# Performance work log

Hardware: AMD Instinct MI355X
Metric: run time of the kernel (lower is better)

The kernel has to match this reference:

```python
import jax, jax.numpy as jnp
import numpy as np

N = 65536          # nodes
E = N * 7          # edges (avg_degree = n_edge_type = 7)
C_IN = 128
C_OUT = 128
N_EDGE_TYPE = 7
N_NODE_TYPE = 5
FEAT = C_IN + N_NODE_TYPE  # 133, channels after one-hot concat


def setup_inputs() -> dict:
    key = jax.random.key(0)
    k1, k2, k3, k4, k5 = jax.random.split(key, 5)
    x = jax.random.normal(k1, (N, C_IN), dtype=jnp.float32)
    edge_idx = jax.random.randint(k2, (2, E), 0, N, dtype=jnp.int64)
    edge_type = jax.random.randint(k3, (E,), 0, N_EDGE_TYPE, dtype=jnp.int64)
    node_type = jax.random.randint(k4, (N,), 0, N_NODE_TYPE, dtype=jnp.int64)
    # uniform init a la module's reset_parameters
    fan_in = 7 * C_IN
    fan_out = 7 * C_OUT
    a = np.sqrt(3.0) * np.sqrt(2.0 / (fan_in + fan_out))
    weights = jax.random.uniform(k5, (N_EDGE_TYPE * FEAT, C_OUT), dtype=jnp.float32,
                                 minval=-a, maxval=a)
    return {"x": x, "edge_idx": edge_idx, "edge_type": edge_type,
            "node_type": node_type, "weights": weights}


def reference(x, edge_idx, edge_type, node_type, weights):
    # one-hot node type concat (n_node_type > 1 branch)
    one_hot = jax.nn.one_hot(node_type, N_NODE_TYPE, dtype=x.dtype)
    xa = jnp.concatenate([x, one_hot], axis=1)          # [N, FEAT]
    row, col = edge_idx[0], edge_idx[1]
    seg = row * N_EDGE_TYPE + edge_type                 # [E]
    gathered = xa[col]                                  # [E, FEAT]
    num_seg = N * N_EDGE_TYPE
    sums = jax.ops.segment_sum(gathered, seg, num_segments=num_seg)
    cnt = jax.ops.segment_sum(jnp.ones((E,), dtype=xa.dtype), seg, num_segments=num_seg)
    col_data = sums / jnp.maximum(cnt, 1.0)[:, None]    # scatter_mean
    # overwrite self-loop slot (last edge type) with node's own features
    self_idx = jnp.arange(N, dtype=jnp.int64) * N_EDGE_TYPE + (N_EDGE_TYPE - 1)
    col_data = col_data.at[self_idx].set(xa)
    out = col_data.reshape(N, N_EDGE_TYPE * FEAT) @ weights  # [N, C_OUT]
    return out
```

## Files before the change

### kernel.cpp

```cpp
#include <hip/hip_runtime.h>
#include <hip/hip_bf16.h>

#define N_NODES 65536
#define N_EDGES (N_NODES * 7)
#define NSEG    (N_NODES * 7)
#define CAP     12
#define ZROW    65536

typedef short short8 __attribute__((ext_vector_type(8)));
typedef float f32x4  __attribute__((ext_vector_type(4)));

__device__ __forceinline__ unsigned short f2bf(float f) {
    return __builtin_bit_cast(unsigned short, (__bf16)f);
}
__device__ __forceinline__ unsigned pack2(float lo, float hi) {
    return (unsigned)f2bf(lo) | ((unsigned)f2bf(hi) << 16);
}
__device__ __forceinline__ float bflo(unsigned d) { return __uint_as_float(d << 16); }
__device__ __forceinline__ float bfhi(unsigned d) { return __uint_as_float(d & 0xffff0000u); }

__global__ __launch_bounds__(256) void k_big(const float* __restrict__ x,
                                             const int* __restrict__ eidx,
                                             const int* __restrict__ etype,
                                             const int* __restrict__ ntype,
                                             const float* __restrict__ W,
                                             unsigned short* __restrict__ xb,
                                             unsigned short* __restrict__ wb,
                                             unsigned* __restrict__ seg32,
                                             unsigned short* __restrict__ scol) {
    int i = blockIdx.x * 256 + threadIdx.x;

    if (i < N_EDGES) {
        int t = etype[i];
        if (t < 6) {
            int r = eidx[i];
            int c = eidx[N_EDGES + i];
            int u = ntype[c];
            unsigned seg = (unsigned)r * 7u + (unsigned)t;
            unsigned inc = 1u | (1u << (7 + 5 * u));
            unsigned old = atomicAdd(&seg32[seg], inc);
            unsigned slot = old & 0x7fu;
            if (slot < CAP) scol[seg * CAP + slot] = (unsigned short)c;
        }
    }

    {
        int row = i >> 4, mm = i & 15;
        const f32x4* p = reinterpret_cast<const f32x4*>(x + (size_t)row * 128 + mm * 8);
        f32x4 v0 = p[0], v1 = p[1];
        uint4 w;
        w.x = pack2(v0[0], v0[1]); w.y = pack2(v0[2], v0[3]);
        w.z = pack2(v1[0], v1[1]); w.w = pack2(v1[2], v1[3]);
        reinterpret_cast<uint4*>(xb)[i] = w;
    }

    if (i < 16) reinterpret_cast<uint4*>(xb + (size_t)ZROW * 128)[i] = (uint4){0u, 0u, 0u, 0u};

    if (i < 143360) {
        int j    = i & 7;
        int lane = (i >> 3) & 63;
        int cb   = (i >> 9) & 7;
        int tkc  = i >> 12;
        int kc   = tkc % 5;
        int t    = tkc / 5;
        int k = kc * 32 + ((lane >> 4) << 3) + j;
        int c = cb * 16 + (lane & 15);
        float v = (k < 133) ? W[(t * 133 + k) * 128 + c] : 0.0f;
        wb[i] = f2bf(v);
    }
}

__global__ __launch_bounds__(512, 4) void k_main(const unsigned short* __restrict__ xb,
                                                 const int* __restrict__ ntype,
                                                 const unsigned* __restrict__ seg32,
                                                 const unsigned short* __restrict__ scol,
                                                 const unsigned short* __restrict__ wb,
                                                 float* __restrict__ out) {
    __shared__ unsigned short sA[7 * 32 * 168];

    const int tid  = threadIdx.x;
    const int lane = tid & 63;
    const int wid  = tid >> 6;
    const int n0   = blockIdx.x * 32;
    const int r    = tid >> 4;
    const int m    = tid & 15;
    const int n    = n0 + r;

    for (int i = tid; i < 7 * 32 * 12; i += 512) {
        int row = i / 12, j = i - row * 12;
        reinterpret_cast<unsigned*>(sA)[row * 84 + 68 + j] = 0u;
    }

    unsigned sv[6], c_t[6];
    uint2 q2[6];
    #pragma unroll
    for (int t = 0; t < 6; ++t) {
        sv[t]  = seg32[n * 7 + t];
        c_t[t] = sv[t] & 0x7fu;
        q2[t]  = *reinterpret_cast<const uint2*>(scol + ((size_t)n * 7 + t) * CAP);
    }

    short8 xA[6], xB[6], xS;
    #pragma unroll
    for (int t = 0; t < 6; ++t) {
        unsigned cA = (c_t[t] >= 1u) ? (q2[t].x & 0xffffu) : (unsigned)ZROW;
        unsigned cB = (c_t[t] >= 2u) ? (q2[t].x >> 16)     : (unsigned)ZROW;
        xA[t] = *reinterpret_cast<const short8*>(xb + (size_t)cA * 128 + m * 8);
        xB[t] = *reinterpret_cast<const short8*>(xb + (size_t)cB * 128 + m * 8);
    }
    xS = *reinterpret_cast<const short8*>(xb + (size_t)n * 128 + m * 8);
    const int ntS = ntype[n];

    #pragma unroll
    for (int t = 0; t < 6; ++t) {
        const unsigned cntv = c_t[t];
        const float inv = (cntv > 1u) ? __builtin_amdgcn_rcpf((float)cntv) : 1.0f;

        uint4 a4 = *reinterpret_cast<const uint4*>(&xA[t]);
        uint4 b4 = *reinterpret_cast<const uint4*>(&xB[t]);
        float a[8];
        a[0] = bflo(a4.x) + bflo(b4.x); a[1] = bfhi(a4.x) + bfhi(b4.x);
        a[2] = bflo(a4.y) + bflo(b4.y); a[3] = bfhi(a4.y) + bfhi(b4.y);
        a[4] = bflo(a4.z) + bflo(b4.z); a[5] = bfhi(a4.z) + bfhi(b4.z);
        a[6] = bflo(a4.w) + bflo(b4.w); a[7] = bfhi(a4.w) + bfhi(b4.w);

        if (cntv >= 3u) {
            const unsigned ce = (cntv < (unsigned)CAP) ? cntv : (unsigned)CAP;
            {
                unsigned c2 = q2[t].y & 0xffffu;
                short8 v = *reinterpret_cast<const short8*>(xb + (size_t)c2 * 128 + m * 8);
                uint4 v4 = *reinterpret_cast<const uint4*>(&v);
                a[0] += bflo(v4.x); a[1] += bfhi(v4.x);
                a[2] += bflo(v4.y); a[3] += bfhi(v4.y);
                a[4] += bflo(v4.z); a[5] += bfhi(v4.z);
                a[6] += bflo(v4.w); a[7] += bfhi(v4.w);
            }
            if (ce >= 4u) {
                unsigned c3 = q2[t].y >> 16;
                short8 v = *reinterpret_cast<const short8*>(xb + (size_t)c3 * 128 + m * 8);
                uint4 v4 = *reinterpret_cast<const uint4*>(&v);
                a[0] += bflo(v4.x); a[1] += bfhi(v4.x);
                a[2] += bflo(v4.y); a[3] += bfhi(v4.y);
                a[4] += bflo(v4.z); a[5] += bfhi(v4.z);
                a[6] += bflo(v4.w); a[7] += bfhi(v4.w);
                const size_t segbase = ((size_t)n * 7 + t) * CAP;
                for (unsigned e = 4; e < ce; ++e) {
                    unsigned c = scol[segbase + e];
                    short8 ve = *reinterpret_cast<const short8*>(xb + (size_t)c * 128 + m * 8);
                    uint4 v4e = *reinterpret_cast<const uint4*>(&ve);
                    a[0] += bflo(v4e.x); a[1] += bfhi(v4e.x);
                    a[2] += bflo(v4e.y); a[3] += bfhi(v4e.y);
                    a[4] += bflo(v4e.z); a[5] += bfhi(v4e.z);
                    a[6] += bflo(v4e.w); a[7] += bfhi(v4e.w);
                }
            }
        }

        uint4 w;
        w.x = pack2(a[0] * inv, a[1] * inv); w.y = pack2(a[2] * inv, a[3] * inv);
        w.z = pack2(a[4] * inv, a[5] * inv); w.w = pack2(a[6] * inv, a[7] * inv);
        *reinterpret_cast<uint4*>(sA + (t * 32 + r) * 168 + m * 8) = w;

        if (m < 4) {
            int i0 = 2 * m, i1 = 2 * m + 1;
            float g0 = (i0 < 5) ? (float)((sv[t] >> (7 + 5 * i0)) & 31u) : 0.f;
            float g1 = (i1 < 5) ? (float)((sv[t] >> (7 + 5 * i1)) & 31u) : 0.f;
            reinterpret_cast<unsigned*>(sA)[(t * 32 + r) * 84 + 64 + m] =
                pack2(g0 * inv, g1 * inv);
        }
    }

    *reinterpret_cast<uint4*>(sA + (6 * 32 + r) * 168 + m * 8) =
        *reinterpret_cast<const uint4*>(&xS);
    if (m < 4) {
        float g0 = (ntS == 2 * m) ? 1.f : 0.f;
        float g1 = (ntS == 2 * m + 1) ? 1.f : 0.f;
        reinterpret_cast<unsigned*>(sA)[(6 * 32 + r) * 84 + 64 + m] = pack2(g0, g1);
    }

    short8 bv[2][5];
    #pragma unroll
    for (int kc = 0; kc < 5; ++kc)
        bv[0][kc] = *reinterpret_cast<const short8*>(
            wb + (((kc * 8 + wid) << 6) + lane) * 8);

    __syncthreads();

    f32x4 acc0 = {0.f, 0.f, 0.f, 0.f};
    f32x4 acc1 = {0.f, 0.f, 0.f, 0.f};
    const int ar = lane & 15;
    const int hi = (lane >> 4) << 3;

    #pragma unroll
    for (int t = 0; t < 7; ++t) {
        const int cur = t & 1, nxt = cur ^ 1;
        if (t < 6) {
            #pragma unroll
            for (int kc = 0; kc < 5; ++kc)
                bv[nxt][kc] = *reinterpret_cast<const short8*>(
                    wb + (((((t + 1) * 5 + kc) * 8 + wid) << 6) + lane) * 8);
        }
        #pragma unroll
        for (int kc = 0; kc < 5; ++kc) {
            short8 a0 = *reinterpret_cast<const short8*>(
                sA + (t * 32 + ar) * 168 + kc * 32 + hi);
            short8 a1 = *reinterpret_cast<const short8*>(
                sA + (t * 32 + 16 + ar) * 168 + kc * 32 + hi);
            acc0 = __builtin_amdgcn_mfma_f32_16x16x32_bf16(a0, bv[cur][kc], acc0, 0, 0, 0);
            acc1 = __builtin_amdgcn_mfma_f32_16x16x32_bf16(a1, bv[cur][kc], acc1, 0, 0, 0);
        }
    }

    const int orow = n0 + ((lane >> 4) << 2);
    const int ocol = (wid << 4) + (lane & 15);
    #pragma unroll
    for (int rr = 0; rr < 4; ++rr) {
        out[(size_t)(orow + rr) * 128 + ocol]      = acc0[rr];
        out[(size_t)(orow + 16 + rr) * 128 + ocol] = acc1[rr];
    }
}


extern "C" void kernel_launch(void* const* d_in, const int* in_sizes, int n_in,
                              void* d_out, int out_size, void* d_ws, size_t ws_size,
                              hipStream_t stream) {
    const float* x     = (const float*)d_in[0];
    const int*   eidx  = (const int*)d_in[1];
    const int*   etype = (const int*)d_in[2];
    const int*   ntype = (const int*)d_in[3];
    const float* W     = (const float*)d_in[4];
    float* out = (float*)d_out;

    unsigned short* xb    = (unsigned short*)d_ws;
    unsigned short* wb    = (unsigned short*)((char*)d_ws + 16777472);
    unsigned*       seg32 = (unsigned*)((char*)d_ws + 17064192);
    unsigned short* scol  = (unsigned short*)((char*)d_ws + 18899200);

    hipMemsetAsync(seg32, 0, NSEG * sizeof(unsigned), stream);
    k_big <<<4096,         256, 0, stream>>>(x, eidx, etype, ntype, W, xb, wb, seg32, scol);
    k_main<<<N_NODES / 32, 512, 0, stream>>>(xb, ntype, seg32, scol, wb, out);
}
```

Before: 81.44 us.

## Split edge-type tiles into two LDS phases to raise occupancy

Shrinks the shared A buffer from 7 to 4 tiles and processes edge types in two halves (types 0-2 plus self, then 3-5), reusing LDS between them behind extra barriers. The second half's gathers are issued before the first MFMA phase so their latency overlaps compute. Launch bounds go from 4 to 6 blocks per CU, and segments with count at most one skip the float unpack/repack. In exchange it adds two __syncthreads, drops the double-buffered weight prefetch, and holds more gathered registers live across the first MFMA phase.

```diff
diff --git a/kernel.cpp b/kernel.cpp
--- a/kernel.cpp
+++ b/kernel.cpp
@@ -70,13 +70,13 @@
     }
 }
 
-__global__ __launch_bounds__(512, 4) void k_main(const unsigned short* __restrict__ xb,
+__global__ __launch_bounds__(512, 6) void k_main(const unsigned short* __restrict__ xb,
                                                  const int* __restrict__ ntype,
                                                  const unsigned* __restrict__ seg32,
                                                  const unsigned short* __restrict__ scol,
                                                  const unsigned short* __restrict__ wb,
                                                  float* __restrict__ out) {
-    __shared__ unsigned short sA[7 * 32 * 168];
+    __shared__ unsigned short sA[4 * 32 * 168];
 
     const int tid  = threadIdx.x;
     const int lane = tid & 63;
@@ -86,7 +86,9 @@
     const int m    = tid & 15;
     const int n    = n0 + r;
 
-    for (int i = tid; i < 7 * 32 * 12; i += 512) {
+    #pragma unroll
+    for (int k2 = 0; k2 < 3; ++k2) {
+        int i = tid + k2 * 512;
         int row = i / 12, j = i - row * 12;
         reinterpret_cast<unsigned*>(sA)[row * 84 + 68 + j] = 0u;
     }
@@ -100,9 +102,9 @@
         q2[t]  = *reinterpret_cast<const uint2*>(scol + ((size_t)n * 7 + t) * CAP);
     }
 
-    short8 xA[6], xB[6], xS;
-    #pragma unroll
-    for (int t = 0; t < 6; ++t) {
+    short8 xA[3], xB[3], xS;
+    #pragma unroll
+    for (int t = 0; t < 3; ++t) {
         unsigned cA = (c_t[t] >= 1u) ? (q2[t].x & 0xffffu) : (unsigned)ZROW;
         unsigned cB = (c_t[t] >= 2u) ? (q2[t].x >> 16)     : (unsigned)ZROW;
         xA[t] = *reinterpret_cast<const short8*>(xb + (size_t)cA * 128 + m * 8);
@@ -111,78 +113,82 @@
     xS = *reinterpret_cast<const short8*>(xb + (size_t)n * 128 + m * 8);
     const int ntS = ntype[n];
 
-    #pragma unroll
-    for (int t = 0; t < 6; ++t) {
+    auto build_tile = [&](int t, int tile, short8 xa, short8 xbv) {
         const unsigned cntv = c_t[t];
         const float inv = (cntv > 1u) ? __builtin_amdgcn_rcpf((float)cntv) : 1.0f;
-
-        uint4 a4 = *reinterpret_cast<const uint4*>(&xA[t]);
-        uint4 b4 = *reinterpret_cast<const uint4*>(&xB[t]);
-        float a[8];
-        a[0] = bflo(a4.x) + bflo(b4.x); a[1] = bfhi(a4.x) + bfhi(b4.x);
-        a[2] = bflo(a4.y) + bflo(b4.y); a[3] = bfhi(a4.y) + bfhi(b4.y);
-        a[4] = bflo(a4.z) + bflo(b4.z); a[5] = bfhi(a4.z) + bfhi(b4.z);
-        a[6] = bflo(a4.w) + bflo(b4.w); a[7] = bfhi(a4.w) + bfhi(b4.w);
-
-        if (cntv >= 3u) {
-            const unsigned ce = (cntv < (unsigned)CAP) ? cntv : (unsigned)CAP;
-            {
-                unsigned c2 = q2[t].y & 0xffffu;
-                short8 v = *reinterpret_cast<const short8*>(xb + (size_t)c2 * 128 + m * 8);
-                uint4 v4 = *reinterpret_cast<const uint4*>(&v);
-                a[0] += bflo(v4.x); a[1] += bfhi(v4.x);
-                a[2] += bflo(v4.y); a[3] += bfhi(v4.y);
-                a[4] += bflo(v4.z); a[5] += bfhi(v4.z);
-                a[6] += bflo(v4.w); a[7] += bfhi(v4.w);
-            }
-            if (ce >= 4u) {
-                unsigned c3 = q2[t].y >> 16;
-                short8 v = *reinterpret_cast<const short8*>(xb + (size_t)c3 * 128 + m * 8);
-                uint4 v4 = *reinterpret_cast<const uint4*>(&v);
-                a[0] += bflo(v4.x); a[1] += bfhi(v4.x);
-                a[2] += bflo(v4.y); a[3] += bfhi(v4.y);
-                a[4] += bflo(v4.z); a[5] += bfhi(v4.z);
-                a[6] += bflo(v4.w); a[7] += bfhi(v4.w);
-                const size_t segbase = ((size_t)n * 7 + t) * CAP;
-                for (unsigned e = 4; e < ce; ++e) {
-                    unsigned c = scol[segbase + e];
-                    short8 ve = *reinterpret_cast<const short8*>(xb + (size_t)c * 128 + m * 8);
-                    uint4 v4e = *reinterpret_cast<const uint4*>(&ve);
-                    a[0] += bflo(v4e.x); a[1] += bfhi(v4e.x);
-                    a[2] += bflo(v4e.y); a[3] += bfhi(v4e.y);
-                    a[4] += bflo(v4e.z); a[5] += bfhi(v4e.z);
-                    a[6] += bflo(v4e.w); a[7] += bfhi(v4e.w);
+        uint4 a4 = *reinterpret_cast<const uint4*>(&xa);
+        uint4 w;
+        if (cntv <= 1u) {
+            w = a4;
+        } else {
+            uint4 b4 = *reinterpret_cast<const uint4*>(&xbv);
+            float a[8];
+            a[0] = bflo(a4.x) + bflo(b4.x); a[1] = bfhi(a4.x) + bfhi(b4.x);
+            a[2] = bflo(a4.y) + bflo(b4.y); a[3] = bfhi(a4.y) + bfhi(b4.y);
+            a[4] = bflo(a4.z) + bflo(b4.z); a[5] = bfhi(a4.z) + bfhi(b4.z);
+            a[6] = bflo(a4.w) + bflo(b4.w); a[7] = bfhi(a4.w) + bfhi(b4.w);
+            if (cntv >= 3u) {
+                const unsigned ce = (cntv < (unsigned)CAP) ? cntv : (unsigned)CAP;
+                {
+                    unsigned c2 = q2[t].y & 0xffffu;
+                    short8 v = *reinterpret_cast<const short8*>(xb + (size_t)c2 * 128 + m * 8);
+                    uint4 v4 = *reinterpret_cast<const uint4*>(&v);
+                    a[0] += bflo(v4.x); a[1] += bfhi(v4.x);
+                    a[2] += bflo(v4.y); a[3] += bfhi(v4.y);
+                    a[4] += bflo(v4.z); a[5] += bfhi(v4.z);
+                    a[6] += bflo(v4.w); a[7] += bfhi(v4.w);
+                }
+                if (ce >= 4u) {
+                    unsigned c3 = q2[t].y >> 16;
+                    short8 v = *reinterpret_cast<const short8*>(xb + (size_t)c3 * 128 + m * 8);
+                    uint4 v4 = *reinterpret_cast<const uint4*>(&v);
+                    a[0] += bflo(v4.x); a[1] += bfhi(v4.x);
+                    a[2] += bflo(v4.y); a[3] += bfhi(v4.y);
+                    a[4] += bflo(v4.z); a[5] += bfhi(v4.z);
+                    a[6] += bflo(v4.w); a[7] += bfhi(v4.w);
+                    const size_t segbase = ((size_t)n * 7 + t) * CAP;
+                    for (unsigned e = 4; e < ce; ++e) {
+                        unsigned c = scol[segbase + e];
+                        short8 ve = *reinterpret_cast<const short8*>(xb + (size_t)c * 128 + m * 8);
+                        uint4 v4e = *reinterpret_cast<const uint4*>(&ve);
+                        a[0] += bflo(v4e.x); a[1] += bfhi(v4e.x);
+                        a[2] += bflo(v4e.y); a[3] += bfhi(v4e.y);
+                        a[4] += bflo(v4e.z); a[5] += bfhi(v4e.z);
+                        a[6] += bflo(v4e.w); a[7] += bfhi(v4e.w);
+                    }
                 }
             }
-        }
-
-        uint4 w;
-        w.x = pack2(a[0] * inv, a[1] * inv); w.y = pack2(a[2] * inv, a[3] * inv);
-        w.z = pack2(a[4] * inv, a[5] * inv); w.w = pack2(a[6] * inv, a[7] * inv);
-        *reinterpret_cast<uint4*>(sA + (t * 32 + r) * 168 + m * 8) = w;
-
+            w.x = pack2(a[0] * inv, a[1] * inv); w.y = pack2(a[2] * inv, a[3] * inv);
+            w.z = pack2(a[4] * inv, a[5] * inv); w.w = pack2(a[6] * inv, a[7] * inv);
+        }
+        *reinterpret_cast<uint4*>(sA + (tile * 32 + r) * 168 + m * 8) = w;
         if (m < 4) {
             int i0 = 2 * m, i1 = 2 * m + 1;
             float g0 = (i0 < 5) ? (float)((sv[t] >> (7 + 5 * i0)) & 31u) : 0.f;
             float g1 = (i1 < 5) ? (float)((sv[t] >> (7 + 5 * i1)) & 31u) : 0.f;
-            reinterpret_cast<unsigned*>(sA)[(t * 32 + r) * 84 + 64 + m] =
+            reinterpret_cast<unsigned*>(sA)[(tile * 32 + r) * 84 + 64 + m] =
                 pack2(g0 * inv, g1 * inv);
         }
-    }
-
-    *reinterpret_cast<uint4*>(sA + (6 * 32 + r) * 168 + m * 8) =
+    };
+
+    #pragma unroll
+    for (int t = 0; t < 3; ++t) build_tile(t, t, xA[t], xB[t]);
+    *reinterpret_cast<uint4*>(sA + (3 * 32 + r) * 168 + m * 8) =
         *reinterpret_cast<const uint4*>(&xS);
     if (m < 4) {
         float g0 = (ntS == 2 * m) ? 1.f : 0.f;
         float g1 = (ntS == 2 * m + 1) ? 1.f : 0.f;
-        reinterpret_cast<unsigned*>(sA)[(6 * 32 + r) * 84 + 64 + m] = pack2(g0, g1);
-    }
-
-    short8 bv[2][5];
-    #pragma unroll
-    for (int kc = 0; kc < 5; ++kc)
-        bv[0][kc] = *reinterpret_cast<const short8*>(
-            wb + (((kc * 8 + wid) << 6) + lane) * 8);
+        reinterpret_cast<unsigned*>(sA)[(3 * 32 + r) * 84 + 64 + m] = pack2(g0, g1);
+    }
+
+    short8 xA2[3], xB2[3];
+    #pragma unroll
+    for (int t = 3; t < 6; ++t) {
+        unsigned cA = (c_t[t] >= 1u) ? (q2[t].x & 0xffffu) : (unsigned)ZROW;
+        unsigned cB = (c_t[t] >= 2u) ? (q2[t].x >> 16)     : (unsigned)ZROW;
+        xA2[t - 3] = *reinterpret_cast<const short8*>(xb + (size_t)cA * 128 + m * 8);
+        xB2[t - 3] = *reinterpret_cast<const short8*>(xb + (size_t)cB * 128 + m * 8);
+    }
 
     __syncthreads();
 
@@ -192,22 +198,47 @@
     const int hi = (lane >> 4) << 3;
 
     #pragma unroll
-    for (int t = 0; t < 7; ++t) {
-        const int cur = t & 1, nxt = cur ^ 1;
-        if (t < 6) {
-            #pragma unroll
-            for (int kc = 0; kc < 5; ++kc)
-                bv[nxt][kc] = *reinterpret_cast<const short8*>(
-                    wb + (((((t + 1) * 5 + kc) * 8 + wid) << 6) + lane) * 8);
-        }
+    for (int i = 0; i < 4; ++i) {
+        const int bt = (i == 3) ? 6 : i;
+        short8 bv[5];
+        #pragma unroll
+        for (int kc = 0; kc < 5; ++kc)
+            bv[kc] = *reinterpret_cast<const short8*>(
+                wb + ((((bt * 5 + kc) * 8 + wid) << 6) + lane) * 8);
         #pragma unroll
         for (int kc = 0; kc < 5; ++kc) {
             short8 a0 = *reinterpret_cast<const short8*>(
-                sA + (t * 32 + ar) * 168 + kc * 32 + hi);
+                sA + (i * 32 + ar) * 168 + kc * 32 + hi);
             short8 a1 = *reinterpret_cast<const short8*>(
-                sA + (t * 32 + 16 + ar) * 168 + kc * 32 + hi);
-            acc0 = __builtin_amdgcn_mfma_f32_16x16x32_bf16(a0, bv[cur][kc], acc0, 0, 0, 0);
-            acc1 = __builtin_amdgcn_mfma_f32_16x16x32_bf16(a1, bv[cur][kc], acc1, 0, 0, 0);
+                sA + (i * 32 + 16 + ar) * 168 + kc * 32 + hi);
+            acc0 = __builtin_amdgcn_mfma_f32_16x16x32_bf16(a0, bv[kc], acc0, 0, 0, 0);
+            acc1 = __builtin_amdgcn_mfma_f32_16x16x32_bf16(a1, bv[kc], acc1, 0, 0, 0);
+        }
+    }
+
+    __syncthreads();
+
+    #pragma unroll
+    for (int t = 0; t < 3; ++t) build_tile(t + 3, t, xA2[t], xB2[t]);
+
+    __syncthreads();
+
+    #pragma unroll
+    for (int i = 0; i < 3; ++i) {
+        const int bt = 3 + i;
+        short8 bv[5];
+        #pragma unroll
+        for (int kc = 0; kc < 5; ++kc)
+            bv[kc] = *reinterpret_cast<const short8*>(
+                wb + ((((bt * 5 + kc) * 8 + wid) << 6) + lane) * 8);
+        #pragma unroll
+        for (int kc = 0; kc < 5; ++kc) {
+            short8 a0 = *reinterpret_cast<const short8*>(
+                sA + (i * 32 + ar) * 168 + kc * 32 + hi);
+            short8 a1 = *reinterpret_cast<const short8*>(
+                sA + (i * 32 + 16 + ar) * 168 + kc * 32 + hi);
+            acc0 = __builtin_amdgcn_mfma_f32_16x16x32_bf16(a0, bv[kc], acc0, 0, 0, 0);
+            acc1 = __builtin_amdgcn_mfma_f32_16x16x32_bf16(a1, bv[kc], acc1, 0, 0, 0);
         }
     }
 
```

New measurement: 108.4 us. 1.33x slower.

## Double-buffer per-edge-type gather tiles in LDS and overlap with MFMA

Applied to the files above, without the earlier changes.

The main kernel now handles 64 nodes per 1024-thread block and keeps only two edge-type slices in LDS instead of all seven. It gathers the next edge type's neighbor features while the current slice feeds the MFMAs. This shrinks LDS per block, which may allow more resident blocks, and interleaves gather latency with compute. It also adds a fast path that skips arithmetic for segments with at most one neighbor. The costs are six extra block-wide barriers, weights reloaded each iteration without prefetch, and a 1024-thread block that must sync across all 16 waves.

```diff
diff --git a/kernel.cpp b/kernel.cpp
--- a/kernel.cpp
+++ b/kernel.cpp
@@ -70,149 +70,152 @@
     }
 }
 
-__global__ __launch_bounds__(512, 4) void k_main(const unsigned short* __restrict__ xb,
-                                                 const int* __restrict__ ntype,
-                                                 const unsigned* __restrict__ seg32,
-                                                 const unsigned short* __restrict__ scol,
-                                                 const unsigned short* __restrict__ wb,
-                                                 float* __restrict__ out) {
-    __shared__ unsigned short sA[7 * 32 * 168];
+__global__ __launch_bounds__(1024, 8) void k_main(const unsigned short* __restrict__ xb,
+                                                  const int* __restrict__ ntype,
+                                                  const unsigned* __restrict__ seg32,
+                                                  const unsigned short* __restrict__ scol,
+                                                  const unsigned short* __restrict__ wb,
+                                                  float* __restrict__ out) {
+    __shared__ unsigned short sA[2 * 64 * 168];
 
     const int tid  = threadIdx.x;
     const int lane = tid & 63;
     const int wid  = tid >> 6;
-    const int n0   = blockIdx.x * 32;
+    const int n0   = blockIdx.x * 64;
     const int r    = tid >> 4;
     const int m    = tid & 15;
     const int n    = n0 + r;
 
-    for (int i = tid; i < 7 * 32 * 12; i += 512) {
+    {
+        int i = tid;
         int row = i / 12, j = i - row * 12;
         reinterpret_cast<unsigned*>(sA)[row * 84 + 68 + j] = 0u;
-    }
-
-    unsigned sv[6], c_t[6];
-    uint2 q2[6];
-    #pragma unroll
-    for (int t = 0; t < 6; ++t) {
-        sv[t]  = seg32[n * 7 + t];
-        c_t[t] = sv[t] & 0x7fu;
-        q2[t]  = *reinterpret_cast<const uint2*>(scol + ((size_t)n * 7 + t) * CAP);
-    }
-
-    short8 xA[6], xB[6], xS;
-    #pragma unroll
-    for (int t = 0; t < 6; ++t) {
-        unsigned cA = (c_t[t] >= 1u) ? (q2[t].x & 0xffffu) : (unsigned)ZROW;
-        unsigned cB = (c_t[t] >= 2u) ? (q2[t].x >> 16)     : (unsigned)ZROW;
-        xA[t] = *reinterpret_cast<const short8*>(xb + (size_t)cA * 128 + m * 8);
-        xB[t] = *reinterpret_cast<const short8*>(xb + (size_t)cB * 128 + m * 8);
-    }
-    xS = *reinterpret_cast<const short8*>(xb + (size_t)n * 128 + m * 8);
-    const int ntS = ntype[n];
-
-    #pragma unroll
-    for (int t = 0; t < 6; ++t) {
-        const unsigned cntv = c_t[t];
+        i = tid + 1024;
+        if (i < 1536) {
+            row = i / 12; j = i - row * 12;
+            reinterpret_cast<unsigned*>(sA)[row * 84 + 68 + j] = 0u;
+        }
+    }
+
+    auto build_gather = [&](int t, int slot, unsigned svt, uint2 q2t) {
+        const unsigned cntv = svt & 0x7fu;
         const float inv = (cntv > 1u) ? __builtin_amdgcn_rcpf((float)cntv) : 1.0f;
-
-        uint4 a4 = *reinterpret_cast<const uint4*>(&xA[t]);
-        uint4 b4 = *reinterpret_cast<const uint4*>(&xB[t]);
-        float a[8];
-        a[0] = bflo(a4.x) + bflo(b4.x); a[1] = bfhi(a4.x) + bfhi(b4.x);
-        a[2] = bflo(a4.y) + bflo(b4.y); a[3] = bfhi(a4.y) + bfhi(b4.y);
-        a[4] = bflo(a4.z) + bflo(b4.z); a[5] = bfhi(a4.z) + bfhi(b4.z);
-        a[6] = bflo(a4.w) + bflo(b4.w); a[7] = bfhi(a4.w) + bfhi(b4.w);
-
-        if (cntv >= 3u) {
-            const unsigned ce = (cntv < (unsigned)CAP) ? cntv : (unsigned)CAP;
-            {
-                unsigned c2 = q2[t].y & 0xffffu;
-                short8 v = *reinterpret_cast<const short8*>(xb + (size_t)c2 * 128 + m * 8);
-                uint4 v4 = *reinterpret_cast<const uint4*>(&v);
-                a[0] += bflo(v4.x); a[1] += bfhi(v4.x);
-                a[2] += bflo(v4.y); a[3] += bfhi(v4.y);
-                a[4] += bflo(v4.z); a[5] += bfhi(v4.z);
-                a[6] += bflo(v4.w); a[7] += bfhi(v4.w);
-            }
-            if (ce >= 4u) {
-                unsigned c3 = q2[t].y >> 16;
-                short8 v = *reinterpret_cast<const short8*>(xb + (size_t)c3 * 128 + m * 8);
-                uint4 v4 = *reinterpret_cast<const uint4*>(&v);
-                a[0] += bflo(v4.x); a[1] += bfhi(v4.x);
-                a[2] += bflo(v4.y); a[3] += bfhi(v4.y);
-                a[4] += bflo(v4.z); a[5] += bfhi(v4.z);
-                a[6] += bflo(v4.w); a[7] += bfhi(v4.w);
-                const size_t segbase = ((size_t)n * 7 + t) * CAP;
-                for (unsigned e = 4; e < ce; ++e) {
-                    unsigned c = scol[segbase + e];
-                    short8 ve = *reinterpret_cast<const short8*>(xb + (size_t)c * 128 + m * 8);
-                    uint4 v4e = *reinterpret_cast<const uint4*>(&ve);
-                    a[0] += bflo(v4e.x); a[1] += bfhi(v4e.x);
-                    a[2] += bflo(v4e.y); a[3] += bfhi(v4e.y);
-                    a[4] += bflo(v4e.z); a[5] += bfhi(v4e.z);
-                    a[6] += bflo(v4e.w); a[7] += bfhi(v4e.w);
+        unsigned cA = (cntv >= 1u) ? (q2t.x & 0xffffu) : (unsigned)ZROW;
+        unsigned cB = (cntv >= 2u) ? (q2t.x >> 16)     : (unsigned)ZROW;
+        short8 xa  = *reinterpret_cast<const short8*>(xb + (size_t)cA * 128 + m * 8);
+        short8 xbv = *reinterpret_cast<const short8*>(xb + (size_t)cB * 128 + m * 8);
+        uint4 a4 = *reinterpret_cast<const uint4*>(&xa);
+        uint4 w;
+        if (cntv <= 1u) {
+            w = a4;
+        } else {
+            uint4 b4 = *reinterpret_cast<const uint4*>(&xbv);
+            float a[8];
+            a[0] = bflo(a4.x) + bflo(b4.x); a[1] = bfhi(a4.x) + bfhi(b4.x);
+            a[2] = bflo(a4.y) + bflo(b4.y); a[3] = bfhi(a4.y) + bfhi(b4.y);
+            a[4] = bflo(a4.z) + bflo(b4.z); a[5] = bfhi(a4.z) + bfhi(b4.z);
+            a[6] = bflo(a4.w) + bflo(b4.w); a[7] = bfhi(a4.w) + bfhi(b4.w);
+            if (cntv >= 3u) {
+                const unsigned ce = (cntv < (unsigned)CAP) ? cntv : (unsigned)CAP;
+                {
+                    unsigned c2 = q2t.y & 0xffffu;
+                    short8 v = *reinterpret_cast<const short8*>(xb + (size_t)c2 * 128 + m * 8);
+                    uint4 v4 = *reinterpret_cast<const uint4*>(&v);
+                    a[0] += bflo(v4.x); a[1] += bfhi(v4.x);
+                    a[2] += bflo(v4.y); a[3] += bfhi(v4.y);
+                    a[4] += bflo(v4.z); a[5] += bfhi(v4.z);
+                    a[6] += bflo(v4.w); a[7] += bfhi(v4.w);
+                }
+                if (ce >= 4u) {
+                    unsigned c3 = q2t.y >> 16;
+                    short8 v = *reinterpret_cast<const short8*>(xb + (size_t)c3 * 128 + m * 8);
+                    uint4 v4 = *reinterpret_cast<const uint4*>(&v);
+                    a[0] += bflo(v4.x); a[1] += bfhi(v4.x);
+                    a[2] += bflo(v4.y); a[3] += bfhi(v4.y);
+                    a[4] += bflo(v4.z); a[5] += bfhi(v4.z);
+                    a[6] += bflo(v4.w); a[7] += bfhi(v4.w);
+                    const size_t segbase = ((size_t)n * 7 + t) * CAP;
+                    for (unsigned e = 4; e < ce; ++e) {
+                        unsigned c = scol[segbase + e];
+                        short8 ve = *reinterpret_cast<const short8*>(xb + (size_t)c * 128 + m * 8);
+                        uint4 v4e = *reinterpret_cast<const uint4*>(&ve);
+                        a[0] += bflo(v4e.x); a[1] += bfhi(v4e.x);
+                        a[2] += bflo(v4e.y); a[3] += bfhi(v4e.y);
+                        a[4] += bflo(v4e.z); a[5] += bfhi(v4e.z);
+                        a[6] += bflo(v4e.w); a[7] += bfhi(v4e.w);
+                    }
                 }
             }
-        }
-
-        uint4 w;
-        w.x = pack2(a[0] * inv, a[1] * inv); w.y = pack2(a[2] * inv, a[3] * inv);
-        w.z = pack2(a[4] * inv, a[5] * inv); w.w = pack2(a[6] * inv, a[7] * inv);
-        *reinterpret_cast<uint4*>(sA + (t * 32 + r) * 168 + m * 8) = w;
-
+            w.x = pack2(a[0] * inv, a[1] * inv); w.y = pack2(a[2] * inv, a[3] * inv);
+            w.z = pack2(a[4] * inv, a[5] * inv); w.w = pack2(a[6] * inv, a[7] * inv);
+        }
+        *reinterpret_cast<uint4*>(sA + (slot * 64 + r) * 168 + m * 8) = w;
         if (m < 4) {
             int i0 = 2 * m, i1 = 2 * m + 1;
-            float g0 = (i0 < 5) ? (float)((sv[t] >> (7 + 5 * i0)) & 31u) : 0.f;
-            float g1 = (i1 < 5) ? (float)((sv[t] >> (7 + 5 * i1)) & 31u) : 0.f;
-            reinterpret_cast<unsigned*>(sA)[(t * 32 + r) * 84 + 64 + m] =
+            float g0 = (i0 < 5) ? (float)((svt >> (7 + 5 * i0)) & 31u) : 0.f;
+            float g1 = (i1 < 5) ? (float)((svt >> (7 + 5 * i1)) & 31u) : 0.f;
+            reinterpret_cast<unsigned*>(sA)[(slot * 64 + r) * 84 + 64 + m] =
                 pack2(g0 * inv, g1 * inv);
         }
-    }
-
-    *reinterpret_cast<uint4*>(sA + (6 * 32 + r) * 168 + m * 8) =
-        *reinterpret_cast<const uint4*>(&xS);
-    if (m < 4) {
-        float g0 = (ntS == 2 * m) ? 1.f : 0.f;
-        float g1 = (ntS == 2 * m + 1) ? 1.f : 0.f;
-        reinterpret_cast<unsigned*>(sA)[(6 * 32 + r) * 84 + 64 + m] = pack2(g0, g1);
-    }
-
-    short8 bv[2][5];
-    #pragma unroll
-    for (int kc = 0; kc < 5; ++kc)
-        bv[0][kc] = *reinterpret_cast<const short8*>(
-            wb + (((kc * 8 + wid) << 6) + lane) * 8);
-
+    };
+
+    auto build_self = [&](int slot) {
+        short8 xs = *reinterpret_cast<const short8*>(xb + (size_t)n * 128 + m * 8);
+        *reinterpret_cast<uint4*>(sA + (slot * 64 + r) * 168 + m * 8) =
+            *reinterpret_cast<const uint4*>(&xs);
+        if (m < 4) {
+            int ntS = ntype[n];
+            float g0 = (ntS == 2 * m) ? 1.f : 0.f;
+            float g1 = (ntS == 2 * m + 1) ? 1.f : 0.f;
+            reinterpret_cast<unsigned*>(sA)[(slot * 64 + r) * 84 + 64 + m] = pack2(g0, g1);
+        }
+    };
+
+    {
+        unsigned svt = seg32[n * 7];
+        uint2 q2t = *reinterpret_cast<const uint2*>(scol + (size_t)n * 7 * CAP);
+        build_gather(0, 0, svt, q2t);
+    }
     __syncthreads();
 
+    const int ch = wid & 7;
+    const int rh = wid >> 3;
+    const int ar = rh * 32 + (lane & 15);
+    const int hi = (lane >> 4) << 3;
     f32x4 acc0 = {0.f, 0.f, 0.f, 0.f};
     f32x4 acc1 = {0.f, 0.f, 0.f, 0.f};
-    const int ar = lane & 15;
-    const int hi = (lane >> 4) << 3;
 
     #pragma unroll
-    for (int t = 0; t < 7; ++t) {
-        const int cur = t & 1, nxt = cur ^ 1;
-        if (t < 6) {
-            #pragma unroll
-            for (int kc = 0; kc < 5; ++kc)
-                bv[nxt][kc] = *reinterpret_cast<const short8*>(
-                    wb + (((((t + 1) * 5 + kc) * 8 + wid) << 6) + lane) * 8);
-        }
+    for (int i = 0; i < 7; ++i) {
+        unsigned svt = 0; uint2 q2t = {0u, 0u};
+        if (i < 5) {
+            svt = seg32[n * 7 + i + 1];
+            q2t = *reinterpret_cast<const uint2*>(scol + ((size_t)n * 7 + i + 1) * CAP);
+        }
+
+        short8 bv[5];
+        #pragma unroll
+        for (int kc = 0; kc < 5; ++kc)
+            bv[kc] = *reinterpret_cast<const short8*>(
+                wb + ((((i * 5 + kc) * 8 + ch) << 6) + lane) * 8);
+        const int base = (i & 1) * 64 * 168;
         #pragma unroll
         for (int kc = 0; kc < 5; ++kc) {
             short8 a0 = *reinterpret_cast<const short8*>(
-                sA + (t * 32 + ar) * 168 + kc * 32 + hi);
+                sA + base + ar * 168 + kc * 32 + hi);
             short8 a1 = *reinterpret_cast<const short8*>(
-                sA + (t * 32 + 16 + ar) * 168 + kc * 32 + hi);
-            acc0 = __builtin_amdgcn_mfma_f32_16x16x32_bf16(a0, bv[cur][kc], acc0, 0, 0, 0);
-            acc1 = __builtin_amdgcn_mfma_f32_16x16x32_bf16(a1, bv[cur][kc], acc1, 0, 0, 0);
-        }
-    }
-
-    const int orow = n0 + ((lane >> 4) << 2);
-    const int ocol = (wid << 4) + (lane & 15);
+                sA + base + (ar + 16) * 168 + kc * 32 + hi);
+            acc0 = __builtin_amdgcn_mfma_f32_16x16x32_bf16(a0, bv[kc], acc0, 0, 0, 0);
+            acc1 = __builtin_amdgcn_mfma_f32_16x16x32_bf16(a1, bv[kc], acc1, 0, 0, 0);
+        }
+
+        if (i < 5)       build_gather(i + 1, (i + 1) & 1, svt, q2t);
+        else if (i == 5) build_self(0);
+        if (i < 6) __syncthreads();
+    }
+
+    const int orow = n0 + rh * 32 + ((lane >> 4) << 2);
+    const int ocol = (ch << 4) + (lane & 15);
     #pragma unroll
     for (int rr = 0; rr < 4; ++rr) {
         out[(size_t)(orow + rr) * 128 + ocol]      = acc0[rr];
@@ -237,6 +240,6 @@
     unsigned short* scol  = (unsigned short*)((char*)d_ws + 18899200);
 
     hipMemsetAsync(seg32, 0, NSEG * sizeof(unsigned), stream);
-    k_big <<<4096,         256, 0, stream>>>(x, eidx, etype, ntype, W, xb, wb, seg32, scol);
-    k_main<<<N_NODES / 32, 512, 0, stream>>>(xb, ntype, seg32, scol, wb, out);
-}
+    k_big <<<4096,          256, 0, stream>>>(x, eidx, etype, ntype, W, xb, wb, seg32, scol);
+    k_main<<<N_NODES / 64, 1024, 0, stream>>>(xb, ntype, seg32, scol, wb, out);
+}
```

Result: slower. 86.02 us (+5.6%).

## Process 64 nodes per block with staged 3-slot LDS tiles and swizzle

Applied to the files above, without the earlier changes.

Doubles the node tile per block from 32 to 64 so each loaded weight fragment feeds four MFMA row-tiles instead of two, halving weight traffic per node. The per-type aggregation tiles are built in three rounds of up to three slots to fit LDS, with syncs between build and MMA phases, and LDS writes and reads use an XOR swizzle to reduce bank conflicts. Each thread now gathers 16 channels per neighbour instead of 8, and single-neighbour segments skip the float accumulation. The trade-off is more barriers, serialised gather and MMA phases with no cross-type prefetch of weights, and fewer blocks in the grid.

```diff
diff --git a/kernel.cpp b/kernel.cpp
--- a/kernel.cpp
+++ b/kernel.cpp
@@ -76,19 +76,22 @@
                                                  const unsigned short* __restrict__ scol,
                                                  const unsigned short* __restrict__ wb,
                                                  float* __restrict__ out) {
-    __shared__ unsigned short sA[7 * 32 * 168];
+    __shared__ unsigned short sA[3 * 64 * 168];
 
     const int tid  = threadIdx.x;
     const int lane = tid & 63;
     const int wid  = tid >> 6;
-    const int n0   = blockIdx.x * 32;
-    const int r    = tid >> 4;
-    const int m    = tid & 15;
+    const int n0   = blockIdx.x * 64;
+    const int r    = tid >> 3;
+    const int m    = tid & 7;
     const int n    = n0 + r;
-
-    for (int i = tid; i < 7 * 32 * 12; i += 512) {
-        int row = i / 12, j = i - row * 12;
-        reinterpret_cast<unsigned*>(sA)[row * 84 + 68 + j] = 0u;
+    const int wswz = ((r >> 3) & 1) << 5;
+
+    if (tid < 192) {
+        uint4 z = {0u, 0u, 0u, 0u};
+        *reinterpret_cast<uint4*>(sA + tid * 168 + 136) = z;
+        *reinterpret_cast<uint4*>(sA + tid * 168 + 144) = z;
+        *reinterpret_cast<uint4*>(sA + tid * 168 + 152) = z;
     }
 
     unsigned sv[6], c_t[6];
@@ -99,124 +102,146 @@
         c_t[t] = sv[t] & 0x7fu;
         q2[t]  = *reinterpret_cast<const uint2*>(scol + ((size_t)n * 7 + t) * CAP);
     }
-
-    short8 xA[6], xB[6], xS;
-    #pragma unroll
-    for (int t = 0; t < 6; ++t) {
-        unsigned cA = (c_t[t] >= 1u) ? (q2[t].x & 0xffffu) : (unsigned)ZROW;
-        unsigned cB = (c_t[t] >= 2u) ? (q2[t].x >> 16)     : (unsigned)ZROW;
-        xA[t] = *reinterpret_cast<const short8*>(xb + (size_t)cA * 128 + m * 8);
-        xB[t] = *reinterpret_cast<const short8*>(xb + (size_t)cB * 128 + m * 8);
-    }
-    xS = *reinterpret_cast<const short8*>(xb + (size_t)n * 128 + m * 8);
     const int ntS = ntype[n];
 
-    #pragma unroll
-    for (int t = 0; t < 6; ++t) {
+    auto addrow = [&](float* f, unsigned col) {
+        const short8* p = reinterpret_cast<const short8*>(xb + (size_t)col * 128 + m * 16);
+        short8 v0 = p[0], v1 = p[1];
+        uint4 u0 = *reinterpret_cast<const uint4*>(&v0);
+        uint4 u1 = *reinterpret_cast<const uint4*>(&v1);
+        f[0] += bflo(u0.x); f[1] += bfhi(u0.x); f[2]  += bflo(u0.y); f[3]  += bfhi(u0.y);
+        f[4] += bflo(u0.z); f[5] += bfhi(u0.z); f[6]  += bflo(u0.w); f[7]  += bfhi(u0.w);
+        f[8] += bflo(u1.x); f[9] += bfhi(u1.x); f[10] += bflo(u1.y); f[11] += bfhi(u1.y);
+        f[12]+= bflo(u1.z); f[13]+= bfhi(u1.z); f[14] += bflo(u1.w); f[15] += bfhi(u1.w);
+    };
+
+    auto build_tile = [&](int t, int tile) {
         const unsigned cntv = c_t[t];
         const float inv = (cntv > 1u) ? __builtin_amdgcn_rcpf((float)cntv) : 1.0f;
-
-        uint4 a4 = *reinterpret_cast<const uint4*>(&xA[t]);
-        uint4 b4 = *reinterpret_cast<const uint4*>(&xB[t]);
-        float a[8];
-        a[0] = bflo(a4.x) + bflo(b4.x); a[1] = bfhi(a4.x) + bfhi(b4.x);
-        a[2] = bflo(a4.y) + bflo(b4.y); a[3] = bfhi(a4.y) + bfhi(b4.y);
-        a[4] = bflo(a4.z) + bflo(b4.z); a[5] = bfhi(a4.z) + bfhi(b4.z);
-        a[6] = bflo(a4.w) + bflo(b4.w); a[7] = bfhi(a4.w) + bfhi(b4.w);
-
-        if (cntv >= 3u) {
-            const unsigned ce = (cntv < (unsigned)CAP) ? cntv : (unsigned)CAP;
-            {
-                unsigned c2 = q2[t].y & 0xffffu;
-                short8 v = *reinterpret_cast<const short8*>(xb + (size_t)c2 * 128 + m * 8);
-                uint4 v4 = *reinterpret_cast<const uint4*>(&v);
-                a[0] += bflo(v4.x); a[1] += bfhi(v4.x);
-                a[2] += bflo(v4.y); a[3] += bfhi(v4.y);
-                a[4] += bflo(v4.z); a[5] += bfhi(v4.z);
-                a[6] += bflo(v4.w); a[7] += bfhi(v4.w);
-            }
-            if (ce >= 4u) {
-                unsigned c3 = q2[t].y >> 16;
-                short8 v = *reinterpret_cast<const short8*>(xb + (size_t)c3 * 128 + m * 8);
-                uint4 v4 = *reinterpret_cast<const uint4*>(&v);
-                a[0] += bflo(v4.x); a[1] += bfhi(v4.x);
-                a[2] += bflo(v4.y); a[3] += bfhi(v4.y);
-                a[4] += bflo(v4.z); a[5] += bfhi(v4.z);
-                a[6] += bflo(v4.w); a[7] += bfhi(v4.w);
-                const size_t segbase = ((size_t)n * 7 + t) * CAP;
-                for (unsigned e = 4; e < ce; ++e) {
-                    unsigned c = scol[segbase + e];
-                    short8 ve = *reinterpret_cast<const short8*>(xb + (size_t)c * 128 + m * 8);
-                    uint4 v4e = *reinterpret_cast<const uint4*>(&ve);
-                    a[0] += bflo(v4e.x); a[1] += bfhi(v4e.x);
-                    a[2] += bflo(v4e.y); a[3] += bfhi(v4e.y);
-                    a[4] += bflo(v4e.z); a[5] += bfhi(v4e.z);
-                    a[6] += bflo(v4e.w); a[7] += bfhi(v4e.w);
+        unsigned cA = (cntv >= 1u) ? (q2[t].x & 0xffffu) : (unsigned)ZROW;
+        unsigned cB = (cntv >= 2u) ? (q2[t].x >> 16)     : (unsigned)ZROW;
+        const short8* pA = reinterpret_cast<const short8*>(xb + (size_t)cA * 128 + m * 16);
+        const short8* pB = reinterpret_cast<const short8*>(xb + (size_t)cB * 128 + m * 16);
+        short8 a0 = pA[0], a1 = pA[1];
+        short8 b0 = pB[0], b1 = pB[1];
+        uint4 w0, w1;
+        if (cntv <= 1u) {
+            w0 = *reinterpret_cast<const uint4*>(&a0);
+            w1 = *reinterpret_cast<const uint4*>(&a1);
+        } else {
+            uint4 ua0 = *reinterpret_cast<const uint4*>(&a0);
+            uint4 ua1 = *reinterpret_cast<const uint4*>(&a1);
+            uint4 ub0 = *reinterpret_cast<const uint4*>(&b0);
+            uint4 ub1 = *reinterpret_cast<const uint4*>(&b1);
+            float f[16];
+            f[0] = bflo(ua0.x)+bflo(ub0.x); f[1] = bfhi(ua0.x)+bfhi(ub0.x);
+            f[2] = bflo(ua0.y)+bflo(ub0.y); f[3] = bfhi(ua0.y)+bfhi(ub0.y);
+            f[4] = bflo(ua0.z)+bflo(ub0.z); f[5] = bfhi(ua0.z)+bfhi(ub0.z);
+            f[6] = bflo(ua0.w)+bflo(ub0.w); f[7] = bfhi(ua0.w)+bfhi(ub0.w);
+            f[8] = bflo(ua1.x)+bflo(ub1.x); f[9] = bfhi(ua1.x)+bfhi(ub1.x);
+            f[10]= bflo(ua1.y)+bflo(ub1.y); f[11]= bfhi(ua1.y)+bfhi(ub1.y);
+            f[12]= bflo(ua1.z)+bflo(ub1.z); f[13]= bfhi(ua1.z)+bfhi(ub1.z);
+            f[14]= bflo(ua1.w)+bflo(ub1.w); f[15]= bfhi(ua1.w)+bfhi(ub1.w);
+            if (cntv >= 3u) {
+                const unsigned ce = (cntv < (unsigned)CAP) ? cntv : (unsigned)CAP;
+                addrow(f, q2[t].y & 0xffffu);
+                if (ce >= 4u) {
+                    addrow(f, q2[t].y >> 16);
+                    const size_t segbase = ((size_t)n * 7 + t) * CAP;
+                    for (unsigned e = 4; e < ce; ++e)
+                        addrow(f, (unsigned)scol[segbase + e]);
                 }
             }
-        }
-
-        uint4 w;
-        w.x = pack2(a[0] * inv, a[1] * inv); w.y = pack2(a[2] * inv, a[3] * inv);
-        w.z = pack2(a[4] * inv, a[5] * inv); w.w = pack2(a[6] * inv, a[7] * inv);
-        *reinterpret_cast<uint4*>(sA + (t * 32 + r) * 168 + m * 8) = w;
-
-        if (m < 4) {
-            int i0 = 2 * m, i1 = 2 * m + 1;
-            float g0 = (i0 < 5) ? (float)((sv[t] >> (7 + 5 * i0)) & 31u) : 0.f;
-            float g1 = (i1 < 5) ? (float)((sv[t] >> (7 + 5 * i1)) & 31u) : 0.f;
-            reinterpret_cast<unsigned*>(sA)[(t * 32 + r) * 84 + 64 + m] =
-                pack2(g0 * inv, g1 * inv);
-        }
-    }
-
-    *reinterpret_cast<uint4*>(sA + (6 * 32 + r) * 168 + m * 8) =
-        *reinterpret_cast<const uint4*>(&xS);
-    if (m < 4) {
-        float g0 = (ntS == 2 * m) ? 1.f : 0.f;
-        float g1 = (ntS == 2 * m + 1) ? 1.f : 0.f;
-        reinterpret_cast<unsigned*>(sA)[(6 * 32 + r) * 84 + 64 + m] = pack2(g0, g1);
-    }
-
-    short8 bv[2][5];
+            w0.x = pack2(f[0]*inv,  f[1]*inv);  w0.y = pack2(f[2]*inv,  f[3]*inv);
+            w0.z = pack2(f[4]*inv,  f[5]*inv);  w0.w = pack2(f[6]*inv,  f[7]*inv);
+            w1.x = pack2(f[8]*inv,  f[9]*inv);  w1.y = pack2(f[10]*inv, f[11]*inv);
+            w1.z = pack2(f[12]*inv, f[13]*inv); w1.w = pack2(f[14]*inv, f[15]*inv);
+        }
+        const int base = (tile * 64 + r) * 168;
+        const int o = (m * 16) ^ wswz;
+        *reinterpret_cast<uint4*>(sA + base + o)     = w0;
+        *reinterpret_cast<uint4*>(sA + base + o + 8) = w1;
+        if (m == 0) {
+            float g0 = (float)((sv[t] >> 7)  & 31u) * inv;
+            float g1 = (float)((sv[t] >> 12) & 31u) * inv;
+            float g2 = (float)((sv[t] >> 17) & 31u) * inv;
+            float g3 = (float)((sv[t] >> 22) & 31u) * inv;
+            float g4 = (float)((sv[t] >> 27) & 31u) * inv;
+            uint4 wo;
+            wo.x = pack2(g0, g1); wo.y = pack2(g2, g3);
+            wo.z = pack2(g4, 0.f); wo.w = 0u;
+            *reinterpret_cast<uint4*>(sA + base + 128) = wo;
+        }
+    };
+
+    auto build_self = [&](int tile) {
+        const short8* p = reinterpret_cast<const short8*>(xb + (size_t)n * 128 + m * 16);
+        short8 s0 = p[0], s1 = p[1];
+        const int base = (tile * 64 + r) * 168;
+        const int o = (m * 16) ^ wswz;
+        *reinterpret_cast<uint4*>(sA + base + o)     = *reinterpret_cast<const uint4*>(&s0);
+        *reinterpret_cast<uint4*>(sA + base + o + 8) = *reinterpret_cast<const uint4*>(&s1);
+        if (m == 0) {
+            uint4 wo;
+            wo.x = pack2((float)(ntS == 0), (float)(ntS == 1));
+            wo.y = pack2((float)(ntS == 2), (float)(ntS == 3));
+            wo.z = pack2((float)(ntS == 4), 0.f);
+            wo.w = 0u;
+            *reinterpret_cast<uint4*>(sA + base + 128) = wo;
+        }
+    };
+
+    const int arl  = lane & 15;
+    const int g8   = (lane >> 4) << 3;
+    const int rswz = ((lane >> 3) & 1) << 5;
+    f32x4 acc[4];
     #pragma unroll
-    for (int kc = 0; kc < 5; ++kc)
-        bv[0][kc] = *reinterpret_cast<const short8*>(
-            wb + (((kc * 8 + wid) << 6) + lane) * 8);
-
-    __syncthreads();
-
-    f32x4 acc0 = {0.f, 0.f, 0.f, 0.f};
-    f32x4 acc1 = {0.f, 0.f, 0.f, 0.f};
-    const int ar = lane & 15;
-    const int hi = (lane >> 4) << 3;
-
-    #pragma unroll
-    for (int t = 0; t < 7; ++t) {
-        const int cur = t & 1, nxt = cur ^ 1;
-        if (t < 6) {
-            #pragma unroll
-            for (int kc = 0; kc < 5; ++kc)
-                bv[nxt][kc] = *reinterpret_cast<const short8*>(
-                    wb + (((((t + 1) * 5 + kc) * 8 + wid) << 6) + lane) * 8);
-        }
+    for (int st = 0; st < 4; ++st) acc[st] = (f32x4){0.f, 0.f, 0.f, 0.f};
+
+    auto marathon = [&](int slot, int bt) {
+        short8 bv[5];
+        #pragma unroll
+        for (int kc = 0; kc < 5; ++kc)
+            bv[kc] = *reinterpret_cast<const short8*>(
+                wb + ((((bt * 5 + kc) * 8 + wid) << 6) + lane) * 8);
         #pragma unroll
         for (int kc = 0; kc < 5; ++kc) {
-            short8 a0 = *reinterpret_cast<const short8*>(
-                sA + (t * 32 + ar) * 168 + kc * 32 + hi);
-            short8 a1 = *reinterpret_cast<const short8*>(
-                sA + (t * 32 + 16 + ar) * 168 + kc * 32 + hi);
-            acc0 = __builtin_amdgcn_mfma_f32_16x16x32_bf16(a0, bv[cur][kc], acc0, 0, 0, 0);
-            acc1 = __builtin_amdgcn_mfma_f32_16x16x32_bf16(a1, bv[cur][kc], acc1, 0, 0, 0);
-        }
-    }
-
-    const int orow = n0 + ((lane >> 4) << 2);
+            const int off = (kc < 4) ? ((kc * 32 + g8) ^ rswz) : (128 + g8);
+            #pragma unroll
+            for (int st = 0; st < 4; ++st) {
+                short8 av = *reinterpret_cast<const short8*>(
+                    sA + (slot * 64 + st * 16 + arl) * 168 + off);
+                acc[st] = __builtin_amdgcn_mfma_f32_16x16x32_bf16(av, bv[kc], acc[st], 0, 0, 0);
+            }
+        }
+    };
+
+    build_tile(0, 0);
+    build_tile(1, 1);
+    build_self(2);
+    __syncthreads();
+    marathon(0, 0); marathon(1, 1); marathon(2, 6);
+    __syncthreads();
+
+    build_tile(2, 0);
+    build_tile(3, 1);
+    __syncthreads();
+    marathon(0, 2); marathon(1, 3);
+    __syncthreads();
+
+    build_tile(4, 0);
+    build_tile(5, 1);
+    __syncthreads();
+    marathon(0, 4); marathon(1, 5);
+
     const int ocol = (wid << 4) + (lane & 15);
+    const int ro   = ((lane >> 4) << 2);
     #pragma unroll
-    for (int rr = 0; rr < 4; ++rr) {
-        out[(size_t)(orow + rr) * 128 + ocol]      = acc0[rr];
-        out[(size_t)(orow + 16 + rr) * 128 + ocol] = acc1[rr];
+    for (int st = 0; st < 4; ++st) {
+        #pragma unroll
+        for (int rr = 0; rr < 4; ++rr) {
+            out[(size_t)(n0 + st * 16 + ro + rr) * 128 + ocol] = acc[st][rr];
+        }
     }
 }
 
@@ -238,5 +263,5 @@
 
     hipMemsetAsync(seg32, 0, NSEG * sizeof(unsigned), stream);
     k_big <<<4096,         256, 0, stream>>>(x, eidx, etype, ntype, W, xb, wb, seg32, scol);
-    k_main<<<N_NODES / 32, 512, 0, stream>>>(xb, ntype, seg32, scol, wb, out);
-}
+    k_main<<<N_NODES / 64, 512, 0, stream>>>(xb, ntype, seg32, scol, wb, out);
+}
```

Result: slower. 83.53 us (+2.6%).
